# Optimization experiments

Hardware: AMD Instinct MI355X
Metric: run time of the kernel (lower is better)

Reference implementation:

```python
import jax, jax.numpy as jnp
import numpy as np

N_ITER = 50  # default n_iter of entmax.entmax_bisect


def entmax_bisect(X, alpha, n_iter=N_ITER):
    """alpha-entmax over the last axis via bisection (entmax package algorithm)."""
    d = X.shape[-1]
    am1 = alpha - 1.0
    inv = 1.0 / am1
    Xa = X * am1

    def p(z):  # clamp(z,0)**(1/(alpha-1)), grad-safe at 0
        return jnp.where(z > 0, jnp.maximum(z, 1e-30) ** inv, 0.0)

    max_val = jnp.max(Xa, axis=-1, keepdims=True)
    tau_lo = max_val - 1.0                       # _gp(1, alpha) = 1
    tau_hi = max_val - (1.0 / d) ** am1          # _gp(1/d, alpha)
    f_lo = jnp.sum(p(Xa - tau_lo), axis=-1, keepdims=True) - 1.0
    dm0 = tau_hi - tau_lo

    def body(carry, _):
        tau_lo, dm, _ = carry
        dm = dm * 0.5
        tau_m = tau_lo + dm
        f_m = jnp.sum(p(Xa - tau_m), axis=-1, keepdims=True) - 1.0
        tau_lo = jnp.where(f_m * f_lo >= 0, tau_m, tau_lo)
        return (tau_lo, dm, tau_m), None

    (_, _, tau_m), _ = jax.lax.scan(body, (tau_lo, dm0, tau_lo), None, length=n_iter)
    pm = p(Xa - tau_m)
    return pm / jnp.sum(pm, axis=-1, keepdims=True)  # ensure_sum_one=True


def setup_inputs() -> dict:
    key = jax.random.key(0)
    ks = jax.random.split(key, 10)
    b, c, e, h = 8, 2048, 64, 8
    s_in = 1.0 / np.sqrt(e)
    s_u = 1.0 / np.sqrt(h * e)
    x = jax.random.normal(ks[0], (b, c, e), jnp.float32)
    Wk = jax.random.normal(ks[1], (h * e, e), jnp.float32) * s_in
    bk = jax.random.normal(ks[2], (h * e,), jnp.float32) * 0.01
    Wq = jax.random.normal(ks[3], (h * e, e), jnp.float32) * s_in
    bq = jax.random.normal(ks[4], (h * e,), jnp.float32) * 0.01
    Wv = jax.random.normal(ks[5], (h * e, e), jnp.float32) * s_in
    bv = jax.random.normal(ks[6], (h * e,), jnp.float32) * 0.01
    Wu = jax.random.normal(ks[7], (e, h * e), jnp.float32) * s_u
    bu = jax.random.normal(ks[8], (e,), jnp.float32) * 0.01
    alpha = jnp.asarray(1.5, jnp.float32)  # learned scalar
    return dict(x=x, alpha=alpha, Wk=Wk, bk=bk, Wq=Wq, bq=bq,
                Wv=Wv, bv=bv, Wu=Wu, bu=bu)


def reference(x, alpha, Wk, bk, Wq, bq, Wv, bv, Wu, bu):
    b, c, e = x.shape
    h = Wk.shape[0] // e
    k = (x @ Wk.T + bk).reshape(b, c, h, e)
    q = (x @ Wq.T + bq).reshape(b, c, h, e)
    v = (x @ Wv.T + bv).reshape(b, c, h, e)
    # dot[b,c,i,j] = sum_h q[b,c,h,i] * k[b,c,h,j] / sqrt(e)   (per-token e x e scores)
    dot = jnp.einsum('bchi,bchj->bcij', q, k) / np.sqrt(e).astype(np.float32)
    att = entmax_bisect(dot, alpha)
    # res[b,c,h,i] = sum_j att[b,c,i,j] * v[b,c,h,j]
    res = jnp.einsum('bcij,bchj->bchi', att, v).reshape(b, c, h * e)
    return res @ Wu.T + bu
```

## Files before the change

kernel.cpp:

```cpp
#include <hip/hip_runtime.h>
#include <math.h>

#define NTOK 16384
#define EDIM 64
#define HHE  512
#define TOKPAD 260

typedef _Float16 half8 __attribute__((ext_vector_type(8)));
typedef __fp16   half2v __attribute__((ext_vector_type(2)));
typedef float    floatx4 __attribute__((ext_vector_type(4)));

__device__ __forceinline__ half8 cvt8(const float4 a, const float4 b) {
    half8 h;
    h[0] = (_Float16)a.x; h[1] = (_Float16)a.y;
    h[2] = (_Float16)a.z; h[3] = (_Float16)a.w;
    h[4] = (_Float16)b.x; h[5] = (_Float16)b.y;
    h[6] = (_Float16)b.z; h[7] = (_Float16)b.w;
    return h;
}

__device__ __forceinline__ float dot2(half2v a, half2v b, float c) {
#if __has_builtin(__builtin_amdgcn_fdot2)
    return __builtin_amdgcn_fdot2(a, b, c, false);
#else
    return fmaf((float)a[0], (float)b[0], fmaf((float)a[1], (float)b[1], c));
#endif
}
__device__ __forceinline__ half2v pk(float x, float y) {
    return __builtin_amdgcn_cvt_pkrtz(x, y);
}
union h2u { half2v h; unsigned int u; };

__device__ __forceinline__ float clamp01(float z) {
    return __builtin_amdgcn_fmed3f(z, 0.0f, 1.0f);
}
__device__ __forceinline__ float pgen(float z, float inv) {
    return z > 0.0f ? exp2f(inv * log2f(fmaxf(z, 1e-30f))) : 0.0f;
}

__global__ __launch_bounds__(256) void cvt_fp16_kernel(
    const float* __restrict__ x,
    const float* __restrict__ Wk, const float* __restrict__ Wq,
    const float* __restrict__ Wv, const float* __restrict__ Wu,
    __fp16* __restrict__ xh, __fp16* __restrict__ wkh,
    __fp16* __restrict__ wqh, __fp16* __restrict__ wvh,
    __fp16* __restrict__ wuh)
{
    const int z = blockIdx.y;
    const float* src; __fp16* dst; int n;
    if      (z == 0) { src = x;  dst = xh;  n = NTOK * EDIM; }
    else if (z == 1) { src = Wk; dst = wkh; n = HHE * EDIM; }
    else if (z == 2) { src = Wq; dst = wqh; n = HHE * EDIM; }
    else if (z == 3) { src = Wv; dst = wvh; n = HHE * EDIM; }
    else             { src = Wu; dst = wuh; n = EDIM * HHE; }
    const int idx = (blockIdx.x * 256 + threadIdx.x) * 8;
    if (idx < n) {
        const float4 a = *(const float4*)(src + idx);
        const float4 b = *(const float4*)(src + idx + 4);
        *(half8*)(dst + idx) = cvt8(a, b);
    }
}

__global__ __launch_bounds__(256) void qkv_attn_out_kernel(
    const __fp16* __restrict__ xh,
    const __fp16* __restrict__ wkh, const float* __restrict__ bk,
    const __fp16* __restrict__ wqh, const float* __restrict__ bq,
    const __fp16* __restrict__ wvh, const float* __restrict__ bv,
    const __fp16* __restrict__ wuh, const float* __restrict__ bu,
    float* __restrict__ out, const float* alpha_p)
{
    __shared__ __align__(16) half2v qT[16 * TOKPAD];
    __shared__ __align__(16) half2v kT[16 * TOKPAD];
    __shared__ __align__(16) half2v vT[16 * TOKPAD];

    const int tid  = threadIdx.x;
    const int lane = tid & 63;
    const int w    = tid >> 6;
    const int tok0 = blockIdx.x * 16;

    const int m    = lane & 15;
    const int quad = lane >> 4;

    const __fp16* xrow = xh + (size_t)(tok0 + m) * EDIM + quad * 8;
    half8 bfr[2];
    bfr[0] = *(const half8*)(xrow);
    bfr[1] = *(const half8*)(xrow + 32);

    #pragma unroll
    for (int uu = 0; uu < 3; ++uu) {
        const int unit = w * 3 + uu;
        const int z    = unit >> 2;
        const int col0 = (unit & 3) * 128;
        const __fp16* W   = (z == 0) ? wkh : (z == 1) ? wqh : wvh;
        const float* bias = (z == 0) ? bk : (z == 1) ? bq : bv;
        half2v* dstT      = (z == 0) ? kT : (z == 1) ? qT : vT;

        #pragma unroll
        for (int ct = 0; ct < 8; ++ct) {
            const int n = col0 + ct * 16 + m;
            const int grow = (z < 2) ? ((n & 7) * 64 + (n >> 3)) : n;
            const __fp16* wrow = W + (size_t)grow * EDIM + quad * 8;
            floatx4 acc = (floatx4){0.f, 0.f, 0.f, 0.f};
            #pragma unroll
            for (int kc = 0; kc < 2; ++kc) {
                const half8 af = *(const half8*)(wrow + kc * 32);
                acc = __builtin_amdgcn_mfma_f32_16x16x32_f16(af, bfr[kc], acc, 0, 0, 0);
            }
            h2u p0, p1;
            if (z < 2) {
                const int hbase = 4 * (quad & 1);
                const int j     = (col0 >> 3) + ct * 2 + (quad >> 1);
                float o0 = acc[0] + bias[(hbase + 0) * 64 + j];
                float o1 = acc[1] + bias[(hbase + 1) * 64 + j];
                float o2 = acc[2] + bias[(hbase + 2) * 64 + j];
                float o3 = acc[3] + bias[(hbase + 3) * 64 + j];
                p0.h = pk(o0, o1);
                p1.h = pk(o2, o3);
                uint2 st; st.x = p0.u; st.y = p1.u;
                *(uint2*)&dstT[m * TOKPAD + j * 4 + 2 * (quad & 1)] = st;
            } else {
                const int nn = col0 + ct * 16 + quad * 4;
                const int h  = nn >> 6;
                const int jj = nn & 63;
                const float4 b4 = *(const float4*)&bias[nn];
                p0.h = pk(acc[0] + b4.x, acc[1] + b4.y);
                p1.h = pk(acc[2] + b4.z, acc[3] + b4.w);
                uint2 st; st.x = p0.u; st.y = p1.u;
                *(uint2*)&dstT[m * TOKPAD + h * 32 + (jj >> 1)] = st;
            }
        }
    }
    __syncthreads();

    const float alpha = alpha_p[0];
    const float am1   = alpha - 1.0f;
    __fp16* resL = (__fp16*)qT;

    for (int i = 0; i < 4; ++i) {
        const int t = w * 4 + i;

        union { half8 h8; half2v h2[4]; } uq;
        uq.h8 = *(const half8*)&qT[t * TOKPAD + lane * 4];

        float row[64];
        #pragma unroll
        for (int j = 0; j < 64; ++j) {
            union { half8 h8; half2v h2[4]; } u;
            u.h8 = *(const half8*)&kT[t * TOKPAD + j * 4];
            float d = dot2(uq.h2[0], u.h2[0], 0.0f);
            d = dot2(uq.h2[1], u.h2[1], d);
            d = dot2(uq.h2[2], u.h2[2], d);
            d = dot2(uq.h2[3], u.h2[3], d);
            row[j] = d;
        }

        const float scale = am1 * 0.125f;
        #pragma unroll
        for (int j = 0; j < 64; ++j) row[j] *= scale;

        float mx = row[0];
        #pragma unroll
        for (int j = 1; j < 64; ++j) mx = fmaxf(mx, row[j]);

        float tau_lo = mx - 1.0f;
        const float tau_hi = mx - exp2f(-6.0f * am1);
        float dm = tau_hi - tau_lo;
        float inv_sum;

        if (am1 == 0.5f) {
            #pragma unroll
            for (int it = 0; it < 6; ++it) {
                dm *= 0.5f;
                const float tau_m = tau_lo + dm;
                float f0 = -1.0f, f1 = 0.0f, f2 = 0.0f, f3 = 0.0f;
                #pragma unroll
                for (int j = 0; j < 64; j += 4) {
                    const float a0 = clamp01(row[j+0] - tau_m);
                    const float a1 = clamp01(row[j+1] - tau_m);
                    const float a2 = clamp01(row[j+2] - tau_m);
                    const float a3 = clamp01(row[j+3] - tau_m);
                    f0 = fmaf(a0, a0, f0); f1 = fmaf(a1, a1, f1);
                    f2 = fmaf(a2, a2, f2); f3 = fmaf(a3, a3, f3);
                }
                const float f = (f0 + f1) + (f2 + f3);
                tau_lo = (f >= 0.0f) ? tau_m : tau_lo;
            }
            float tau = tau_lo;
            #pragma unroll
            for (int it = 0; it < 2; ++it) {
                float f0 = -1.0f, f1 = 0.0f, f2 = 0.0f, f3 = 0.0f;
                float s0 = 0.0f, s1 = 0.0f, s2 = 0.0f, s3 = 0.0f;
                #pragma unroll
                for (int j = 0; j < 64; j += 4) {
                    const float a0 = clamp01(row[j+0] - tau);
                    const float a1 = clamp01(row[j+1] - tau);
                    const float a2 = clamp01(row[j+2] - tau);
                    const float a3 = clamp01(row[j+3] - tau);
                    f0 = fmaf(a0, a0, f0); f1 = fmaf(a1, a1, f1);
                    f2 = fmaf(a2, a2, f2); f3 = fmaf(a3, a3, f3);
                    s0 += a0; s1 += a1; s2 += a2; s3 += a3;
                }
                const float f = (f0 + f1) + (f2 + f3);
                const float s = ((s0 + s1) + (s2 + s3)) + 1e-20f;
                tau = tau + fmaxf(f, 0.0f) / (s + s);
            }
            float s0 = 0.0f, s1 = 0.0f;
            #pragma unroll
            for (int j = 0; j < 64; j += 2) {
                float a0 = clamp01(row[j+0] - tau);
                float a1 = clamp01(row[j+1] - tau);
                a0 *= a0; a1 *= a1;
                row[j+0] = a0; row[j+1] = a1;
                s0 += a0; s1 += a1;
            }
            inv_sum = 1.0f / (s0 + s1);
        } else {
            const float inv = 1.0f / am1;
            float tau_m = tau_lo;
            float f_lo = -1.0f;
            #pragma unroll
            for (int j = 0; j < 64; ++j) f_lo += pgen(row[j] - tau_lo, inv);
            for (int it = 0; it < 30; ++it) {
                dm *= 0.5f;
                tau_m = tau_lo + dm;
                float f = -1.0f;
                #pragma unroll
                for (int j = 0; j < 64; ++j) f += pgen(row[j] - tau_m, inv);
                tau_lo = (f * f_lo >= 0.0f) ? tau_m : tau_lo;
            }
            float s = 0.0f;
            #pragma unroll
            for (int j = 0; j < 64; ++j) {
                const float pm = pgen(row[j] - tau_m, inv);
                row[j] = pm;
                s += pm;
            }
            inv_sum = 1.0f / s;
        }

        half2v p2[32];
        #pragma unroll
        for (int ii = 0; ii < 32; ++ii) p2[ii] = pk(row[2 * ii], row[2 * ii + 1]);

        float acc[8];
        #pragma unroll
        for (int h = 0; h < 8; ++h) {
            float a0 = 0.0f, a1 = 0.0f;
            #pragma unroll
            for (int jc = 0; jc < 8; ++jc) {
                union { half8 h8; half2v h2[4]; } u;
                u.h8 = *(const half8*)&vT[t * TOKPAD + h * 32 + jc * 4];
                a0 = dot2(p2[jc * 4 + 0], u.h2[0], a0);
                a1 = dot2(p2[jc * 4 + 1], u.h2[1], a1);
                a0 = dot2(p2[jc * 4 + 2], u.h2[2], a0);
                a1 = dot2(p2[jc * 4 + 3], u.h2[3], a1);
            }
            acc[h] = a0 + a1;
        }
        #pragma unroll
        for (int h = 0; h < 8; ++h)
            resL[t * 520 + h * 64 + lane] = (__fp16)(acc[h] * inv_sum);
    }
    __syncthreads();

    {
        floatx4 oacc = (floatx4){0.f, 0.f, 0.f, 0.f};
        const __fp16* rrow = resL + (size_t)m * 520 + quad * 8;
        const __fp16* wrow = wuh + (size_t)(w * 16 + m) * HHE + quad * 8;
        #pragma unroll
        for (int kc = 0; kc < 16; ++kc) {
            const half8 bf = *(const half8*)(rrow + kc * 32);
            const half8 af = *(const half8*)(wrow + kc * 32);
            oacc = __builtin_amdgcn_mfma_f32_16x16x32_f16(af, bf, oacc, 0, 0, 0);
        }
        const int tok = tok0 + m;
        const int col = w * 16 + quad * 4;
        const float4 b4 = *(const float4*)&bu[col];
        float4 o;
        o.x = oacc[0] + b4.x;
        o.y = oacc[1] + b4.y;
        o.z = oacc[2] + b4.z;
        o.w = oacc[3] + b4.w;
        *(float4*)&out[(size_t)tok * 64 + col] = o;
    }
}

extern "C" void kernel_launch(void* const* d_in, const int* in_sizes, int n_in,
                              void* d_out, int out_size, void* d_ws, size_t ws_size,
                              hipStream_t stream)
{
    const float* x     = (const float*)d_in[0];
    const float* alpha = (const float*)d_in[1];
    const float* Wk    = (const float*)d_in[2];
    const float* bk    = (const float*)d_in[3];
    const float* Wq    = (const float*)d_in[4];
    const float* bq    = (const float*)d_in[5];
    const float* Wv    = (const float*)d_in[6];
    const float* bv    = (const float*)d_in[7];
    const float* Wu    = (const float*)d_in[8];
    const float* bu    = (const float*)d_in[9];
    float* out = (float*)d_out;

    __fp16* xh   = (__fp16*)d_ws;
    __fp16* wkh  = xh  + (size_t)NTOK * EDIM;
    __fp16* wqh  = wkh + (size_t)HHE * EDIM;
    __fp16* wvh  = wqh + (size_t)HHE * EDIM;
    __fp16* wuh  = wvh + (size_t)HHE * EDIM;

    cvt_fp16_kernel<<<dim3(512, 5), 256, 0, stream>>>(
        x, Wk, Wq, Wv, Wu, xh, wkh, wqh, wvh, wuh);
    qkv_attn_out_kernel<<<NTOK / 16, 256, 0, stream>>>(
        xh, wkh, bk, wqh, bq, wvh, bv, wuh, bu, out, alpha);
}
```

Baseline: 158.2 us.

## Halve tokens per block, fold x conversion and score scale into fused kernel

Each block now handles 8 tokens instead of 16, doubling the grid, and every wave processes 2 tokens of the entmax stage instead of 4. The separate fp32-to-fp16 pass over x is dropped; x is loaded and converted directly inside the fused kernel. The (alpha-1)/8 scale is folded into Wq during weight conversion and into the q bias, which removes the per-score multiply. The MFMA tiles stay 16 wide, so half of the projection and output work is computed and thrown away, a cost accepted in exchange for more blocks, less LDS per block and less serial entmax work per wave. The change also pairs the score dot products, uses a tree max reduction and an rcp approximation, and replaces fmed3 clamps with fmax.

```diff
diff --git a/kernel.cpp b/kernel.cpp
--- a/kernel.cpp
+++ b/kernel.cpp
@@ -4,6 +4,7 @@
 #define NTOK 16384
 #define EDIM 64
 #define HHE  512
+#define TPB  8
 #define TOKPAD 260
 
 typedef _Float16 half8 __attribute__((ext_vector_type(8)));
@@ -31,60 +32,67 @@
 }
 union h2u { half2v h; unsigned int u; };
 
-__device__ __forceinline__ float clamp01(float z) {
-    return __builtin_amdgcn_fmed3f(z, 0.0f, 1.0f);
-}
 __device__ __forceinline__ float pgen(float z, float inv) {
     return z > 0.0f ? exp2f(inv * log2f(fmaxf(z, 1e-30f))) : 0.0f;
 }
 
 __global__ __launch_bounds__(256) void cvt_fp16_kernel(
-    const float* __restrict__ x,
     const float* __restrict__ Wk, const float* __restrict__ Wq,
     const float* __restrict__ Wv, const float* __restrict__ Wu,
-    __fp16* __restrict__ xh, __fp16* __restrict__ wkh,
-    __fp16* __restrict__ wqh, __fp16* __restrict__ wvh,
-    __fp16* __restrict__ wuh)
+    __fp16* __restrict__ wkh, __fp16* __restrict__ wqh,
+    __fp16* __restrict__ wvh, __fp16* __restrict__ wuh,
+    const float* alpha_p)
 {
     const int z = blockIdx.y;
-    const float* src; __fp16* dst; int n;
-    if      (z == 0) { src = x;  dst = xh;  n = NTOK * EDIM; }
-    else if (z == 1) { src = Wk; dst = wkh; n = HHE * EDIM; }
-    else if (z == 2) { src = Wq; dst = wqh; n = HHE * EDIM; }
-    else if (z == 3) { src = Wv; dst = wvh; n = HHE * EDIM; }
-    else             { src = Wu; dst = wuh; n = EDIM * HHE; }
+    const float* src; __fp16* dst;
+    float s = 1.0f;
+    if      (z == 0) { src = Wk; dst = wkh; }
+    else if (z == 1) { src = Wq; dst = wqh; s = (alpha_p[0] - 1.0f) * 0.125f; }
+    else if (z == 2) { src = Wv; dst = wvh; }
+    else             { src = Wu; dst = wuh; }
     const int idx = (blockIdx.x * 256 + threadIdx.x) * 8;
-    if (idx < n) {
-        const float4 a = *(const float4*)(src + idx);
-        const float4 b = *(const float4*)(src + idx + 4);
-        *(half8*)(dst + idx) = cvt8(a, b);
-    }
+    float4 a = *(const float4*)(src + idx);
+    float4 b = *(const float4*)(src + idx + 4);
+    a.x *= s; a.y *= s; a.z *= s; a.w *= s;
+    b.x *= s; b.y *= s; b.z *= s; b.w *= s;
+    *(half8*)(dst + idx) = cvt8(a, b);
 }
 
 __global__ __launch_bounds__(256) void qkv_attn_out_kernel(
-    const __fp16* __restrict__ xh,
+    const float* __restrict__ x,
     const __fp16* __restrict__ wkh, const float* __restrict__ bk,
     const __fp16* __restrict__ wqh, const float* __restrict__ bq,
     const __fp16* __restrict__ wvh, const float* __restrict__ bv,
     const __fp16* __restrict__ wuh, const float* __restrict__ bu,
     float* __restrict__ out, const float* alpha_p)
 {
-    __shared__ __align__(16) half2v qT[16 * TOKPAD];
-    __shared__ __align__(16) half2v kT[16 * TOKPAD];
-    __shared__ __align__(16) half2v vT[16 * TOKPAD];
+    __shared__ __align__(16) half2v qT[TPB * TOKPAD];
+    __shared__ __align__(16) half2v kT[TPB * TOKPAD];
+    __shared__ __align__(16) half2v vT[TPB * TOKPAD];
 
     const int tid  = threadIdx.x;
     const int lane = tid & 63;
     const int w    = tid >> 6;
-    const int tok0 = blockIdx.x * 16;
+    const int tok0 = blockIdx.x * TPB;
 
     const int m    = lane & 15;
     const int quad = lane >> 4;
 
-    const __fp16* xrow = xh + (size_t)(tok0 + m) * EDIM + quad * 8;
+    const float alpha = alpha_p[0];
+    const float am1   = alpha - 1.0f;
+    const float s_q   = am1 * 0.125f;
+
+    const int trow = tok0 + m < NTOK - 1 ? tok0 + m : NTOK - 1;
+    const float* xrow = x + (size_t)trow * EDIM + quad * 8;
     half8 bfr[2];
-    bfr[0] = *(const half8*)(xrow);
-    bfr[1] = *(const half8*)(xrow + 32);
+    {
+        const float4 a0 = *(const float4*)(xrow);
+        const float4 a1 = *(const float4*)(xrow + 4);
+        const float4 a2 = *(const float4*)(xrow + 32);
+        const float4 a3 = *(const float4*)(xrow + 36);
+        bfr[0] = cvt8(a0, a1);
+        bfr[1] = cvt8(a2, a3);
+    }
 
     #pragma unroll
     for (int uu = 0; uu < 3; ++uu) {
@@ -94,6 +102,7 @@
         const __fp16* W   = (z == 0) ? wkh : (z == 1) ? wqh : wvh;
         const float* bias = (z == 0) ? bk : (z == 1) ? bq : bv;
         half2v* dstT      = (z == 0) ? kT : (z == 1) ? qT : vT;
+        const float bs    = (z == 1) ? s_q : 1.0f;
 
         #pragma unroll
         for (int ct = 0; ct < 8; ++ct) {
@@ -110,14 +119,16 @@
             if (z < 2) {
                 const int hbase = 4 * (quad & 1);
                 const int j     = (col0 >> 3) + ct * 2 + (quad >> 1);
-                float o0 = acc[0] + bias[(hbase + 0) * 64 + j];
-                float o1 = acc[1] + bias[(hbase + 1) * 64 + j];
-                float o2 = acc[2] + bias[(hbase + 2) * 64 + j];
-                float o3 = acc[3] + bias[(hbase + 3) * 64 + j];
+                float o0 = fmaf(bias[(hbase + 0) * 64 + j], bs, acc[0]);
+                float o1 = fmaf(bias[(hbase + 1) * 64 + j], bs, acc[1]);
+                float o2 = fmaf(bias[(hbase + 2) * 64 + j], bs, acc[2]);
+                float o3 = fmaf(bias[(hbase + 3) * 64 + j], bs, acc[3]);
                 p0.h = pk(o0, o1);
                 p1.h = pk(o2, o3);
-                uint2 st; st.x = p0.u; st.y = p1.u;
-                *(uint2*)&dstT[m * TOKPAD + j * 4 + 2 * (quad & 1)] = st;
+                if (m < TPB) {
+                    uint2 st; st.x = p0.u; st.y = p1.u;
+                    *(uint2*)&dstT[m * TOKPAD + j * 4 + 2 * (quad & 1)] = st;
+                }
             } else {
                 const int nn = col0 + ct * 16 + quad * 4;
                 const int h  = nn >> 6;
@@ -125,47 +136,58 @@
                 const float4 b4 = *(const float4*)&bias[nn];
                 p0.h = pk(acc[0] + b4.x, acc[1] + b4.y);
                 p1.h = pk(acc[2] + b4.z, acc[3] + b4.w);
-                uint2 st; st.x = p0.u; st.y = p1.u;
-                *(uint2*)&dstT[m * TOKPAD + h * 32 + (jj >> 1)] = st;
+                if (m < TPB) {
+                    uint2 st; st.x = p0.u; st.y = p1.u;
+                    *(uint2*)&dstT[m * TOKPAD + h * 32 + (jj >> 1)] = st;
+                }
             }
         }
     }
     __syncthreads();
 
-    const float alpha = alpha_p[0];
-    const float am1   = alpha - 1.0f;
     __fp16* resL = (__fp16*)qT;
 
-    for (int i = 0; i < 4; ++i) {
-        const int t = w * 4 + i;
+    for (int i = 0; i < 2; ++i) {
+        const int t = w * 2 + i;
 
         union { half8 h8; half2v h2[4]; } uq;
         uq.h8 = *(const half8*)&qT[t * TOKPAD + lane * 4];
 
         float row[64];
         #pragma unroll
-        for (int j = 0; j < 64; ++j) {
-            union { half8 h8; half2v h2[4]; } u;
-            u.h8 = *(const half8*)&kT[t * TOKPAD + j * 4];
-            float d = dot2(uq.h2[0], u.h2[0], 0.0f);
-            d = dot2(uq.h2[1], u.h2[1], d);
-            d = dot2(uq.h2[2], u.h2[2], d);
-            d = dot2(uq.h2[3], u.h2[3], d);
-            row[j] = d;
-        }
-
-        const float scale = am1 * 0.125f;
-        #pragma unroll
-        for (int j = 0; j < 64; ++j) row[j] *= scale;
-
-        float mx = row[0];
-        #pragma unroll
-        for (int j = 1; j < 64; ++j) mx = fmaxf(mx, row[j]);
+        for (int j = 0; j < 64; j += 2) {
+            union { half8 h8; half2v h2[4]; } u0, u1;
+            u0.h8 = *(const half8*)&kT[t * TOKPAD + j * 4];
+            u1.h8 = *(const half8*)&kT[t * TOKPAD + (j + 1) * 4];
+            float d0 = dot2(uq.h2[0], u0.h2[0], 0.0f);
+            float d1 = dot2(uq.h2[0], u1.h2[0], 0.0f);
+            d0 = dot2(uq.h2[1], u0.h2[1], d0);
+            d1 = dot2(uq.h2[1], u1.h2[1], d1);
+            d0 = dot2(uq.h2[2], u0.h2[2], d0);
+            d1 = dot2(uq.h2[2], u1.h2[2], d1);
+            d0 = dot2(uq.h2[3], u0.h2[3], d0);
+            d1 = dot2(uq.h2[3], u1.h2[3], d1);
+            row[j] = d0; row[j + 1] = d1;
+        }
+
+        float m0 = fmaxf(row[0], row[1]);
+        float m1 = fmaxf(row[2], row[3]);
+        float m2 = fmaxf(row[4], row[5]);
+        float m3 = fmaxf(row[6], row[7]);
+        #pragma unroll
+        for (int j = 8; j < 64; j += 8) {
+            m0 = fmaxf(m0, fmaxf(row[j + 0], row[j + 1]));
+            m1 = fmaxf(m1, fmaxf(row[j + 2], row[j + 3]));
+            m2 = fmaxf(m2, fmaxf(row[j + 4], row[j + 5]));
+            m3 = fmaxf(m3, fmaxf(row[j + 6], row[j + 7]));
+        }
+        const float mx = fmaxf(fmaxf(m0, m1), fmaxf(m2, m3));
 
         float tau_lo = mx - 1.0f;
         const float tau_hi = mx - exp2f(-6.0f * am1);
         float dm = tau_hi - tau_lo;
         float inv_sum;
+        half2v p2[32];
 
         if (am1 == 0.5f) {
             #pragma unroll
@@ -175,10 +197,10 @@
                 float f0 = -1.0f, f1 = 0.0f, f2 = 0.0f, f3 = 0.0f;
                 #pragma unroll
                 for (int j = 0; j < 64; j += 4) {
-                    const float a0 = clamp01(row[j+0] - tau_m);
-                    const float a1 = clamp01(row[j+1] - tau_m);
-                    const float a2 = clamp01(row[j+2] - tau_m);
-                    const float a3 = clamp01(row[j+3] - tau_m);
+                    const float a0 = fmaxf(row[j + 0] - tau_m, 0.0f);
+                    const float a1 = fmaxf(row[j + 1] - tau_m, 0.0f);
+                    const float a2 = fmaxf(row[j + 2] - tau_m, 0.0f);
+                    const float a3 = fmaxf(row[j + 3] - tau_m, 0.0f);
                     f0 = fmaf(a0, a0, f0); f1 = fmaf(a1, a1, f1);
                     f2 = fmaf(a2, a2, f2); f3 = fmaf(a3, a3, f3);
                 }
@@ -192,25 +214,25 @@
                 float s0 = 0.0f, s1 = 0.0f, s2 = 0.0f, s3 = 0.0f;
                 #pragma unroll
                 for (int j = 0; j < 64; j += 4) {
-                    const float a0 = clamp01(row[j+0] - tau);
-                    const float a1 = clamp01(row[j+1] - tau);
-                    const float a2 = clamp01(row[j+2] - tau);
-                    const float a3 = clamp01(row[j+3] - tau);
+                    const float a0 = fmaxf(row[j + 0] - tau, 0.0f);
+                    const float a1 = fmaxf(row[j + 1] - tau, 0.0f);
+                    const float a2 = fmaxf(row[j + 2] - tau, 0.0f);
+                    const float a3 = fmaxf(row[j + 3] - tau, 0.0f);
                     f0 = fmaf(a0, a0, f0); f1 = fmaf(a1, a1, f1);
                     f2 = fmaf(a2, a2, f2); f3 = fmaf(a3, a3, f3);
                     s0 += a0; s1 += a1; s2 += a2; s3 += a3;
                 }
                 const float f = (f0 + f1) + (f2 + f3);
                 const float s = ((s0 + s1) + (s2 + s3)) + 1e-20f;
-                tau = tau + fmaxf(f, 0.0f) / (s + s);
+                tau = tau + fmaxf(f, 0.0f) * __builtin_amdgcn_rcpf(s + s);
             }
             float s0 = 0.0f, s1 = 0.0f;
             #pragma unroll
             for (int j = 0; j < 64; j += 2) {
-                float a0 = clamp01(row[j+0] - tau);
-                float a1 = clamp01(row[j+1] - tau);
+                float a0 = fmaxf(row[j + 0] - tau, 0.0f);
+                float a1 = fmaxf(row[j + 1] - tau, 0.0f);
                 a0 *= a0; a1 *= a1;
-                row[j+0] = a0; row[j+1] = a1;
+                row[j + 0] = a0; row[j + 1] = a1;
                 s0 += a0; s1 += a1;
             }
             inv_sum = 1.0f / (s0 + s1);
@@ -238,7 +260,6 @@
             inv_sum = 1.0f / s;
         }
 
-        half2v p2[32];
         #pragma unroll
         for (int ii = 0; ii < 32; ++ii) p2[ii] = pk(row[2 * ii], row[2 * ii + 1]);
 
@@ -265,7 +286,8 @@
 
     {
         floatx4 oacc = (floatx4){0.f, 0.f, 0.f, 0.f};
-        const __fp16* rrow = resL + (size_t)m * 520 + quad * 8;
+        const int mm = m & 7;
+        const __fp16* rrow = resL + (size_t)mm * 520 + quad * 8;
         const __fp16* wrow = wuh + (size_t)(w * 16 + m) * HHE + quad * 8;
         #pragma unroll
         for (int kc = 0; kc < 16; ++kc) {
@@ -273,15 +295,17 @@
             const half8 af = *(const half8*)(wrow + kc * 32);
             oacc = __builtin_amdgcn_mfma_f32_16x16x32_f16(af, bf, oacc, 0, 0, 0);
         }
-        const int tok = tok0 + m;
-        const int col = w * 16 + quad * 4;
-        const float4 b4 = *(const float4*)&bu[col];
-        float4 o;
-        o.x = oacc[0] + b4.x;
-        o.y = oacc[1] + b4.y;
-        o.z = oacc[2] + b4.z;
-        o.w = oacc[3] + b4.w;
-        *(float4*)&out[(size_t)tok * 64 + col] = o;
+        if (m < TPB) {
+            const int tok = tok0 + m;
+            const int col = w * 16 + quad * 4;
+            const float4 b4 = *(const float4*)&bu[col];
+            float4 o;
+            o.x = oacc[0] + b4.x;
+            o.y = oacc[1] + b4.y;
+            o.z = oacc[2] + b4.z;
+            o.w = oacc[3] + b4.w;
+            *(float4*)&out[(size_t)tok * 64 + col] = o;
+        }
     }
 }
 
@@ -301,14 +325,13 @@
     const float* bu    = (const float*)d_in[9];
     float* out = (float*)d_out;
 
-    __fp16* xh   = (__fp16*)d_ws;
-    __fp16* wkh  = xh  + (size_t)NTOK * EDIM;
+    __fp16* wkh  = (__fp16*)d_ws;
     __fp16* wqh  = wkh + (size_t)HHE * EDIM;
     __fp16* wvh  = wqh + (size_t)HHE * EDIM;
     __fp16* wuh  = wvh + (size_t)HHE * EDIM;
 
-    cvt_fp16_kernel<<<dim3(512, 5), 256, 0, stream>>>(
-        x, Wk, Wq, Wv, Wu, xh, wkh, wqh, wvh, wuh);
-    qkv_attn_out_kernel<<<NTOK / 16, 256, 0, stream>>>(
-        xh, wkh, bk, wqh, bq, wvh, bv, wuh, bu, out, alpha);
-}
+    cvt_fp16_kernel<<<dim3(16, 4), 256, 0, stream>>>(
+        Wk, Wq, Wv, Wu, wkh, wqh, wvh, wuh, alpha);
+    qkv_attn_out_kernel<<<NTOK / TPB, 256, 0, stream>>>(
+        x, wkh, bk, wqh, bq, wvh, bv, wuh, bu, out, alpha);
+}
```

Measured after the change: 182.7 us. 1.16x slower.
